# Kernel optimization log

Measured on AMD Instinct MI355X. Metric: run time of the kernel, lower is better.

Reference implementation:

```python
import jax, jax.numpy as jnp
import numpy as np

N, F, E, G = 50000, 128, 1600000, 64
CH = [16, 32, 64, 128, 256]
K = 3
EPS = 1e-5


def setup_inputs() -> dict:
    key = jax.random.key(0)
    ks = jax.random.split(key, 16)
    inp = {}
    inp["x"] = jax.random.normal(ks[0], (N, F), jnp.float32)
    inp["edge_weight"] = jax.random.uniform(ks[1], (E,), jnp.float32)
    inp["edge_index"] = jax.random.randint(ks[2], (2, E), 0, N)
    inp["batch_index"] = jnp.sort(jax.random.randint(ks[3], (N,), 0, G))
    dims = [F] + CH
    i = 4
    for l in range(5):
        fi, fo = dims[l], dims[l + 1]
        inp[f"W{l+1}"] = jax.random.normal(ks[i], (K, fi, fo), jnp.float32) / np.sqrt(K * fi)
        i += 1
        inp[f"b{l+1}"] = jnp.zeros((fo,), jnp.float32)
        if l < 4:  # no BN after the 5th conv
            inp[f"g{l+1}"] = jnp.ones((fo,), jnp.float32)
            inp[f"be{l+1}"] = jnp.zeros((fo,), jnp.float32)
    inp["Wd"] = jax.random.normal(ks[i], (2 * CH[-1], 4), jnp.float32) / np.sqrt(2 * CH[-1])
    inp["bd"] = jnp.zeros((4,), jnp.float32)
    inp["num_graphs"] = G
    return inp


def _bn(h, g, b):
    m = jnp.mean(h, axis=0)
    v = jnp.mean(jnp.square(h - m), axis=0)  # biased variance (torch training mode)
    return g * (h - m) / jnp.sqrt(v + EPS) + b


def reference(x, edge_weight, W1, b1, g1, be1, W2, b2, g2, be2, W3, b3, g3, be3,
              W4, b4, g4, be4, W5, b5, Wd, bd, edge_index, batch_index, num_graphs):
    n = x.shape[0]
    row, col = edge_index[0], edge_index[1]
    # sym-normalized Laplacian, lambda_max=2 -> scaled L_hat has zero diagonal,
    # off-diagonal = -w * deg^-1/2[row] * deg^-1/2[col]
    deg = jax.ops.segment_sum(edge_weight, row, num_segments=n)
    dinv = jnp.where(deg > 0, jax.lax.rsqrt(jnp.where(deg > 0, deg, 1.0)), 0.0)
    norm = -edge_weight * dinv[row] * dinv[col]

    def prop(z):  # L_hat @ z via sparse gather/scatter over edges
        return jax.ops.segment_sum(norm[:, None] * z[col], row, num_segments=n)

    def cheb(z, W, b):  # T0=z, T1=L z, T2=2 L T1 - T0
        t1 = prop(z)
        out = z @ W[0] + t1 @ W[1]
        t2 = 2.0 * prop(t1) - z
        return out + t2 @ W[2] + b

    h = _bn(jax.nn.softplus(cheb(x, W1, b1)), g1, be1)
    h = _bn(jax.nn.softplus(cheb(h, W2, b2)), g2, be2)
    h = _bn(jax.nn.softplus(cheb(h, W3, b3)), g3, be3)
    h = _bn(jax.nn.softplus(cheb(h, W4, b4)), g4, be4)
    h = cheb(h, W5, b5)

    mx = jax.ops.segment_max(h, batch_index, num_segments=num_graphs)
    mx = jnp.where(jnp.isfinite(mx), mx, 0.0)  # guard empty segments
    cnt = jax.ops.segment_sum(jnp.ones((n,), h.dtype), batch_index, num_segments=num_graphs)
    mean = jax.ops.segment_sum(h, batch_index, num_segments=num_graphs) / jnp.maximum(cnt, 1.0)[:, None]
    pooled = jnp.concatenate([mx, mean], axis=1)  # [G, 512]
    logits = pooled @ Wd + bd
    return jax.nn.log_softmax(logits, axis=-1)
```

## Files before the change

kernel.cpp:

```cpp
#include <hip/hip_runtime.h>
#include <cmath>

#define NN 50000
#define NE 1600000
#define NG 64
#define CAP 96

typedef __attribute__((ext_vector_type(8))) short short8_t;
typedef __attribute__((ext_vector_type(4))) float floatx4;
typedef __attribute__((ext_vector_type(4))) unsigned short us4;

static __device__ __forceinline__ float softplusf(float x) {
    return fmaxf(x, 0.0f) + log1pf(expf(-fabsf(x)));
}

static __device__ __forceinline__ float bf2f(unsigned short u) {
    return __uint_as_float(((unsigned)u) << 16);
}
static __device__ __forceinline__ unsigned short f2bf(float x) {
    unsigned u = __float_as_uint(x);
    unsigned t = (u >> 16) & 1u;
    return (unsigned short)((u + 0x7FFFu + t) >> 16);
}

static __device__ __forceinline__ void split_bf16(float x, unsigned short& hi, unsigned short& lo) {
    unsigned u = __float_as_uint(x);
    unsigned hb = u & 0xFFFF0000u;
    hi = (unsigned short)(hb >> 16);
    float r = x - __uint_as_float(hb);
    lo = f2bf(r);
}

__global__ void k_slot(const int* __restrict__ row, const int* __restrict__ col,
                       const float* __restrict__ w,
                       int* __restrict__ cnt, int2* __restrict__ slots) {
    int e = blockIdx.x * blockDim.x + threadIdx.x;
    if (e < NE) {
        int r = row[e];
        int k = atomicAdd(&cnt[r], 1);
        k = min(k, CAP - 1);
        slots[(size_t)r * CAP + k] = make_int2(col[e], __float_as_int(w[e]));
    }
}

__global__ __launch_bounds__(256) void k_degsum(const int* __restrict__ cnt,
                                                const int2* __restrict__ slots,
                                                float* __restrict__ dinv) {
    int tid = threadIdx.x;
    int lane = tid & 15;
    int node = blockIdx.x * 16 + (tid >> 4);
    if (node >= NN) return;
    int e = cnt[node];
    const int2* base = slots + (size_t)node * CAP;
    float s = 0.0f;
    for (int k = lane; k < e; k += 16) s += __int_as_float(base[k].y);
#pragma unroll
    for (int m = 8; m >= 1; m >>= 1) s += __shfl_xor(s, m);
    if (lane == 0) dinv[node] = (s > 0.0f) ? rsqrtf(s) : 0.0f;
}

__global__ __launch_bounds__(256) void k_rescale(const int* __restrict__ cnt,
                                                 int2* __restrict__ slots,
                                                 const float* __restrict__ dinv) {
    int tid = threadIdx.x;
    int lane = tid & 15;
    int node = blockIdx.x * 16 + (tid >> 4);
    if (node >= NN) return;
    int e = cnt[node];
    float dr = dinv[node];
    int2* base = slots + (size_t)node * CAP;
    for (int k = lane; k < e; k += 16) {
        int2 s = base[k];
        float wv = __int_as_float(s.y);
        base[k].y = __float_as_int(-wv * dr * dinv[s.x]);
    }
}

__global__ void k_wcat1(const float* __restrict__ W1, float* __restrict__ wc) {
    int i = blockIdx.x * blockDim.x + threadIdx.x;
    if (i < 128 * 48) {
        int k = i / 48, j = i - k * 48;
        float v;
        if (j < 16)      v = W1[k * 16 + j] - W1[2 * 2048 + k * 16 + j];
        else if (j < 32) v = W1[2048 + k * 16 + (j - 16)];
        else             v = W1[2 * 2048 + k * 16 + (j - 32)];
        wc[i] = v;
    }
}

__global__ void k_wsplit(const float* __restrict__ W, int K, int N,
                         unsigned short* __restrict__ hiT, unsigned short* __restrict__ loT) {
    int idx = blockIdx.x * 256 + threadIdx.x;
    if (idx < K * N) {
        int k = idx / N, n = idx - k * N;
        unsigned short h, l;
        split_bf16(W[idx], h, l);
        hiT[(size_t)n * K + k] = h;
        loT[(size_t)n * K + k] = l;
    }
}

#define ASTR 40

__global__ __launch_bounds__(256, 2) void k_gemm_mfma_f32A(
    const float* __restrict__ A, int lda,
    const unsigned short* __restrict__ BhiT,
    const unsigned short* __restrict__ BloT,
    unsigned short* __restrict__ C, int ldc,
    int M, int K, int Ncol)
{
    __shared__ unsigned short Ah[128 * ASTR];
    __shared__ unsigned short Al[128 * ASTR];
    __shared__ unsigned short Bh[128 * ASTR];
    __shared__ unsigned short Bl[128 * ASTR];

    const int tid = threadIdx.x;
    const int lane = tid & 63;
    const int wave = tid >> 6;
    const int wm = wave >> 1, wn = wave & 1;
    const int quad = lane >> 4, l16 = lane & 15;
    const int bm = blockIdx.y * 128, bn = blockIdx.x * 128;
    const int srow = tid >> 1;
    const int skq  = (tid & 1) * 16;

    floatx4 acc[4][4];
#pragma unroll
    for (int i = 0; i < 4; ++i)
#pragma unroll
        for (int j = 0; j < 4; ++j) acc[i][j] = (floatx4){0.f, 0.f, 0.f, 0.f};

    for (int k0 = 0; k0 < K; k0 += 32) {
        float4 a0 = make_float4(0, 0, 0, 0), a1 = a0, a2 = a0, a3 = a0;
        const int ga = bm + srow;
        if (ga < M) {
            const float* Ap = A + (size_t)ga * lda + k0 + skq;
            a0 = *(const float4*)(Ap + 0);
            a1 = *(const float4*)(Ap + 4);
            a2 = *(const float4*)(Ap + 8);
            a3 = *(const float4*)(Ap + 12);
        }
        uint4 bh0 = make_uint4(0, 0, 0, 0), bh1 = bh0, bl0 = bh0, bl1 = bh0;
        const int gb = bn + srow;
        if (gb < Ncol) {
            const unsigned short* ph = BhiT + (size_t)gb * K + k0 + skq;
            const unsigned short* pl = BloT + (size_t)gb * K + k0 + skq;
            bh0 = *(const uint4*)(ph);
            bh1 = *(const uint4*)(ph + 8);
            bl0 = *(const uint4*)(pl);
            bl1 = *(const uint4*)(pl + 8);
        }
        __attribute__((aligned(16))) unsigned short ah[16], al[16];
        const float av[16] = {a0.x, a0.y, a0.z, a0.w, a1.x, a1.y, a1.z, a1.w,
                              a2.x, a2.y, a2.z, a2.w, a3.x, a3.y, a3.z, a3.w};
#pragma unroll
        for (int i = 0; i < 16; ++i) split_bf16(av[i], ah[i], al[i]);

        __syncthreads();
        *(uint4*)&Ah[srow * ASTR + skq]     = *(const uint4*)&ah[0];
        *(uint4*)&Ah[srow * ASTR + skq + 8] = *(const uint4*)&ah[8];
        *(uint4*)&Al[srow * ASTR + skq]     = *(const uint4*)&al[0];
        *(uint4*)&Al[srow * ASTR + skq + 8] = *(const uint4*)&al[8];
        *(uint4*)&Bh[srow * ASTR + skq]     = bh0;
        *(uint4*)&Bh[srow * ASTR + skq + 8] = bh1;
        *(uint4*)&Bl[srow * ASTR + skq]     = bl0;
        *(uint4*)&Bl[srow * ASTR + skq + 8] = bl1;
        __syncthreads();

        short8_t afh[4], afl[4], bfh[4], bfl[4];
#pragma unroll
        for (int t = 0; t < 4; ++t) {
            const int m = wm * 64 + t * 16 + l16;
            afh[t] = *(const short8_t*)&Ah[m * ASTR + quad * 8];
            afl[t] = *(const short8_t*)&Al[m * ASTR + quad * 8];
            const int n = wn * 64 + t * 16 + l16;
            bfh[t] = *(const short8_t*)&Bh[n * ASTR + quad * 8];
            bfl[t] = *(const short8_t*)&Bl[n * ASTR + quad * 8];
        }
#pragma unroll
        for (int i = 0; i < 4; ++i)
#pragma unroll
            for (int j = 0; j < 4; ++j) {
                acc[i][j] = __builtin_amdgcn_mfma_f32_16x16x32_bf16(afh[i], bfh[j], acc[i][j], 0, 0, 0);
                acc[i][j] = __builtin_amdgcn_mfma_f32_16x16x32_bf16(afh[i], bfl[j], acc[i][j], 0, 0, 0);
                acc[i][j] = __builtin_amdgcn_mfma_f32_16x16x32_bf16(afl[i], bfh[j], acc[i][j], 0, 0, 0);
            }
    }

#pragma unroll
    for (int j = 0; j < 4; ++j) {
        const int col = bn + wn * 64 + j * 16 + l16;
        if (col >= Ncol) continue;
#pragma unroll
        for (int i = 0; i < 4; ++i) {
#pragma unroll
            for (int r = 0; r < 4; ++r) {
                const int row = bm + wm * 64 + i * 16 + quad * 4 + r;
                if (row >= M) continue;
                C[(size_t)row * ldc + col] = f2bf(acc[i][j][r]);
            }
        }
    }
}

__global__ __launch_bounds__(256, 2) void k_gemm_mfma_bf(
    const unsigned short* __restrict__ A, int lda,
    const unsigned short* __restrict__ BhiT,
    const unsigned short* __restrict__ BloT,
    void* __restrict__ Cv, int ldc,
    int M, int K, int Ncol,
    const float* __restrict__ bias, int act, int c_f32)
{
    __shared__ unsigned short Ah[128 * ASTR];
    __shared__ unsigned short Bh[128 * ASTR];
    __shared__ unsigned short Bl[128 * ASTR];

    const int tid = threadIdx.x;
    const int lane = tid & 63;
    const int wave = tid >> 6;
    const int wm = wave >> 1, wn = wave & 1;
    const int quad = lane >> 4, l16 = lane & 15;
    const int bm = blockIdx.y * 128, bn = blockIdx.x * 128;
    const int srow = tid >> 1;
    const int skq  = (tid & 1) * 16;

    floatx4 acc[4][4];
#pragma unroll
    for (int i = 0; i < 4; ++i)
#pragma unroll
        for (int j = 0; j < 4; ++j) acc[i][j] = (floatx4){0.f, 0.f, 0.f, 0.f};

    for (int k0 = 0; k0 < K; k0 += 32) {
        uint4 a0 = make_uint4(0, 0, 0, 0), a1 = a0;
        const int ga = bm + srow;
        if (ga < M) {
            const unsigned short* Ap = A + (size_t)ga * lda + k0 + skq;
            a0 = *(const uint4*)(Ap);
            a1 = *(const uint4*)(Ap + 8);
        }
        uint4 bh0 = make_uint4(0, 0, 0, 0), bh1 = bh0, bl0 = bh0, bl1 = bh0;
        const int gb = bn + srow;
        if (gb < Ncol) {
            const unsigned short* ph = BhiT + (size_t)gb * K + k0 + skq;
            const unsigned short* pl = BloT + (size_t)gb * K + k0 + skq;
            bh0 = *(const uint4*)(ph);
            bh1 = *(const uint4*)(ph + 8);
            bl0 = *(const uint4*)(pl);
            bl1 = *(const uint4*)(pl + 8);
        }
        __syncthreads();
        *(uint4*)&Ah[srow * ASTR + skq]     = a0;
        *(uint4*)&Ah[srow * ASTR + skq + 8] = a1;
        *(uint4*)&Bh[srow * ASTR + skq]     = bh0;
        *(uint4*)&Bh[srow * ASTR + skq + 8] = bh1;
        *(uint4*)&Bl[srow * ASTR + skq]     = bl0;
        *(uint4*)&Bl[srow * ASTR + skq + 8] = bl1;
        __syncthreads();

        short8_t afh[4], bfh[4], bfl[4];
#pragma unroll
        for (int t = 0; t < 4; ++t) {
            const int m = wm * 64 + t * 16 + l16;
            afh[t] = *(const short8_t*)&Ah[m * ASTR + quad * 8];
            const int n = wn * 64 + t * 16 + l16;
            bfh[t] = *(const short8_t*)&Bh[n * ASTR + quad * 8];
            bfl[t] = *(const short8_t*)&Bl[n * ASTR + quad * 8];
        }
#pragma unroll
        for (int i = 0; i < 4; ++i)
#pragma unroll
            for (int j = 0; j < 4; ++j) {
                acc[i][j] = __builtin_amdgcn_mfma_f32_16x16x32_bf16(afh[i], bfh[j], acc[i][j], 0, 0, 0);
                acc[i][j] = __builtin_amdgcn_mfma_f32_16x16x32_bf16(afh[i], bfl[j], acc[i][j], 0, 0, 0);
            }
    }

    float* Cf = (float*)Cv;
    unsigned short* Cb = (unsigned short*)Cv;
#pragma unroll
    for (int j = 0; j < 4; ++j) {
        const int col = bn + wn * 64 + j * 16 + l16;
        if (col >= Ncol) continue;
        const float bv = bias ? bias[col] : 0.0f;
#pragma unroll
        for (int i = 0; i < 4; ++i) {
#pragma unroll
            for (int r = 0; r < 4; ++r) {
                const int row = bm + wm * 64 + i * 16 + quad * 4 + r;
                if (row >= M) continue;
                float v = acc[i][j][r] + bv;
                if (act) v = softplusf(v);
                if (c_f32) Cf[(size_t)row * ldc + col] = v;
                else       Cb[(size_t)row * ldc + col] = f2bf(v);
            }
        }
    }
}

__global__ __launch_bounds__(256) void k_gemm(
    const unsigned short* __restrict__ A, int lda,
    const float* __restrict__ B, int ldb,
    unsigned short* __restrict__ C, int ldc,
    int M, int K, int Ncol,
    const float* __restrict__ bias, int act)
{
    __shared__ float As[16][128];
    __shared__ float Bs[16][128];
    const int tid = threadIdx.x;
    const int tx = tid & 15;
    const int ty = tid >> 4;
    const int bm = blockIdx.y * 128;
    const int bn = blockIdx.x * 128;
    const int arow = tid >> 1;
    const int akq = (tid & 1) * 8;
    const int bkr = tid >> 4;
    const int bcq = (tid & 15) * 8;

    float acc[8][8];
#pragma unroll
    for (int i = 0; i < 8; ++i)
#pragma unroll
        for (int j = 0; j < 8; ++j) acc[i][j] = 0.0f;

    for (int k0 = 0; k0 < K; k0 += 16) {
        uint4 ald = make_uint4(0, 0, 0, 0);
        int gr = bm + arow;
        if (gr < M) ald = *(const uint4*)(A + (size_t)gr * lda + k0 + akq);
        float4 b0 = make_float4(0, 0, 0, 0), b1 = make_float4(0, 0, 0, 0);
        int cb = bn + bcq;
        const float* Bp = B + (k0 + bkr) * ldb;
        if (cb < Ncol)     b0 = *(const float4*)(Bp + cb);
        if (cb + 4 < Ncol) b1 = *(const float4*)(Bp + cb + 4);
        __syncthreads();
        const unsigned short* au = (const unsigned short*)&ald;
#pragma unroll
        for (int i = 0; i < 8; ++i) As[akq + i][arow] = bf2f(au[i]);
        *(float4*)&Bs[bkr][bcq] = b0;
        *(float4*)&Bs[bkr][bcq + 4] = b1;
        __syncthreads();
#pragma unroll
        for (int kk = 0; kk < 16; ++kk) {
            float a[8], b[8];
            float4 t;
            t = *(const float4*)&As[kk][ty * 4];      a[0] = t.x; a[1] = t.y; a[2] = t.z; a[3] = t.w;
            t = *(const float4*)&As[kk][64 + ty * 4]; a[4] = t.x; a[5] = t.y; a[6] = t.z; a[7] = t.w;
            t = *(const float4*)&Bs[kk][tx * 4];      b[0] = t.x; b[1] = t.y; b[2] = t.z; b[3] = t.w;
            t = *(const float4*)&Bs[kk][64 + tx * 4]; b[4] = t.x; b[5] = t.y; b[6] = t.z; b[7] = t.w;
#pragma unroll
            for (int i = 0; i < 8; ++i)
#pragma unroll
                for (int j = 0; j < 8; ++j)
                    acc[i][j] = fmaf(a[i], b[j], acc[i][j]);
        }
    }
#pragma unroll
    for (int i = 0; i < 8; ++i) {
        int r = bm + ((i < 4) ? (ty * 4 + i) : (64 + ty * 4 + i - 4));
        if (r >= M) continue;
#pragma unroll
        for (int j = 0; j < 8; ++j) {
            int cl = bn + ((j < 4) ? (tx * 4 + j) : (64 + tx * 4 + j - 4));
            if (cl >= Ncol) continue;
            float v = acc[i][j];
            if (bias) v += bias[cl];
            if (act) v = softplusf(v);
            C[(size_t)r * ldc + cl] = f2bf(v);
        }
    }
}

__global__ __launch_bounds__(256) void k_prop(
    const int* __restrict__ cnt, const int2* __restrict__ slots,
    const unsigned short* __restrict__ z, int zld, int zoff,
    unsigned short* __restrict__ out, int outld, int ooff,
    int ltw, float alpha,
    const unsigned short* __restrict__ add1, int a1ld, int a1off, float c1,
    const unsigned short* __restrict__ add2, int a2ld, int a2off,
    const float* __restrict__ bias, int act)
{
    const int T = 1 << ltw;
    const int lane = threadIdx.x & (T - 1);
    const int node = blockIdx.x * (256 >> ltw) + (threadIdx.x >> ltw);
    if (node >= NN) return;
    const int f4 = lane * 4;
    const int e = cnt[node];
    const int2* base = slots + (size_t)node * CAP;
    float ax = 0, ay = 0, az = 0, aw = 0;
    float bx = 0, by = 0, bz = 0, bw = 0;
    const unsigned short* zp = z + zoff + f4;
    int p = 0;
    for (; p + 4 <= e; p += 4) {
        int2 s0 = base[p + 0], s1 = base[p + 1], s2 = base[p + 2], s3 = base[p + 3];
        float w0 = __int_as_float(s0.y), w1 = __int_as_float(s1.y);
        float w2 = __int_as_float(s2.y), w3 = __int_as_float(s3.y);
        const us4 z0 = *(const us4*)(zp + (size_t)s0.x * zld);
        const us4 z1 = *(const us4*)(zp + (size_t)s1.x * zld);
        const us4 z2 = *(const us4*)(zp + (size_t)s2.x * zld);
        const us4 z3 = *(const us4*)(zp + (size_t)s3.x * zld);
        ax = fmaf(w0, bf2f(z0.x), ax); ay = fmaf(w0, bf2f(z0.y), ay);
        az = fmaf(w0, bf2f(z0.z), az); aw = fmaf(w0, bf2f(z0.w), aw);
        bx = fmaf(w1, bf2f(z1.x), bx); by = fmaf(w1, bf2f(z1.y), by);
        bz = fmaf(w1, bf2f(z1.z), bz); bw = fmaf(w1, bf2f(z1.w), bw);
        ax = fmaf(w2, bf2f(z2.x), ax); ay = fmaf(w2, bf2f(z2.y), ay);
        az = fmaf(w2, bf2f(z2.z), az); aw = fmaf(w2, bf2f(z2.w), aw);
        bx = fmaf(w3, bf2f(z3.x), bx); by = fmaf(w3, bf2f(z3.y), by);
        bz = fmaf(w3, bf2f(z3.z), bz); bw = fmaf(w3, bf2f(z3.w), bw);
    }
    for (; p < e; ++p) {
        int2 s = base[p];
        float wv = __int_as_float(s.y);
        const us4 zv = *(const us4*)(zp + (size_t)s.x * zld);
        ax = fmaf(wv, bf2f(zv.x), ax); ay = fmaf(wv, bf2f(zv.y), ay);
        az = fmaf(wv, bf2f(zv.z), az); aw = fmaf(wv, bf2f(zv.w), aw);
    }
    ax += bx; ay += by; az += bz; aw += bw;
    ax *= alpha; ay *= alpha; az *= alpha; aw *= alpha;
    if (add1) {
        const us4 t = *(const us4*)(add1 + (size_t)node * a1ld + a1off + f4);
        ax = fmaf(c1, bf2f(t.x), ax); ay = fmaf(c1, bf2f(t.y), ay);
        az = fmaf(c1, bf2f(t.z), az); aw = fmaf(c1, bf2f(t.w), aw);
    }
    if (add2) {
        const us4 t = *(const us4*)(add2 + (size_t)node * a2ld + a2off + f4);
        ax += bf2f(t.x); ay += bf2f(t.y); az += bf2f(t.z); aw += bf2f(t.w);
    }
    if (bias) {
        const float4 t = *(const float4*)(bias + f4);
        ax += t.x; ay += t.y; az += t.z; aw += t.w;
    }
    if (act) { ax = softplusf(ax); ay = softplusf(ay); az = softplusf(az); aw = softplusf(aw); }
    us4 o;
    o.x = f2bf(ax); o.y = f2bf(ay); o.z = f2bf(az); o.w = f2bf(aw);
    *(us4*)(out + (size_t)node * outld + ooff + f4) = o;
}

__global__ __launch_bounds__(256) void k_bnstats(const unsigned short* __restrict__ h, int ld, int lc,
                                                 float* __restrict__ stats) {
    const int C = 1 << lc;
    const int tid = threadIdx.x;
    const int c = tid & (C - 1);
    const int rpb = 256 >> lc;
    int r = blockIdx.x * rpb + (tid >> lc);
    const int stride = gridDim.x * rpb;
    float s = 0.0f, q = 0.0f;
    for (; r < NN; r += stride) {
        float v = bf2f(h[(size_t)r * ld + c]);
        s += v;
        q = fmaf(v, v, q);
    }
    __shared__ float shs[256], shq[256];
    shs[tid] = s; shq[tid] = q;
    __syncthreads();
    for (int o = 128; o >= C; o >>= 1) {
        if (tid < o) { shs[tid] += shs[tid + o]; shq[tid] += shq[tid + o]; }
        __syncthreads();
    }
    if (tid < C) {
        atomicAdd(&stats[c], shs[tid]);
        atomicAdd(&stats[128 + c], shq[tid]);
    }
}

__global__ void k_bnapply(unsigned short* __restrict__ h, int ld, int lc,
                          const float* __restrict__ stats,
                          const float* __restrict__ g, const float* __restrict__ be) {
    int idx = blockIdx.x * 256 + threadIdx.x;
    if (idx >= (NN << lc)) return;
    int c = idx & ((1 << lc) - 1);
    int r = idx >> lc;
    const float invN = 1.0f / (float)NN;
    float m = stats[c] * invN;
    float var = fmaf(stats[128 + c], invN, -m * m);
    var = fmaxf(var, 0.0f);
    float inv = rsqrtf(var + 1e-5f);
    float v = bf2f(h[(size_t)r * ld + c]);
    h[(size_t)r * ld + c] = f2bf(fmaf(g[c] * inv, v - m, be[c]));
}

static __device__ __forceinline__ int lower_bound_dev(const int* __restrict__ b, int val) {
    int lo = 0, hi = NN;
    while (lo < hi) {
        int mid = (lo + hi) >> 1;
        if (b[mid] < val) lo = mid + 1; else hi = mid;
    }
    return lo;
}

__global__ void k_gbounds(const int* __restrict__ batch, int* __restrict__ gb) {
    int g = threadIdx.x;
    if (g <= NG) gb[g] = (g == NG) ? NN : lower_bound_dev(batch, g);
}

__global__ __launch_bounds__(256) void k_pool1(const float* __restrict__ h,
                                               const int* __restrict__ gb,
                                               float* __restrict__ partial) {
    int g = blockIdx.y;
    int j = blockIdx.x;
    int start = gb[g], end = gb[g + 1];
    int len = end - start;
    int chunk = (len + 15) >> 4;
    int s = start + j * chunk;
    int e = min(s + chunk, end);
    int c = threadIdx.x;
    float mx = -INFINITY, sum = 0.0f;
    for (int r = s; r < e; ++r) {
        float v = h[(size_t)r * 256 + c];
        mx = fmaxf(mx, v);
        sum += v;
    }
    size_t base = ((size_t)(g * 16 + j)) * 512;
    partial[base + c] = mx;
    partial[base + 256 + c] = sum;
}

__global__ __launch_bounds__(256) void k_pool2d(const float* __restrict__ partial,
                                                const int* __restrict__ gb,
                                                const float* __restrict__ Wd,
                                                const float* __restrict__ bd,
                                                float* __restrict__ out) {
    __shared__ float pl[512];
    __shared__ float red[4][256];
    int g = blockIdx.x;
    int c = threadIdx.x;
    float mx = -INFINITY, sum = 0.0f;
#pragma unroll
    for (int j = 0; j < 16; ++j) {
        size_t base = ((size_t)(g * 16 + j)) * 512;
        mx = fmaxf(mx, partial[base + c]);
        sum += partial[base + 256 + c];
    }
    int len = gb[g + 1] - gb[g];
    pl[c] = (len > 0) ? mx : 0.0f;
    pl[256 + c] = sum / fmaxf((float)len, 1.0f);
    __syncthreads();
    float p[4] = {0, 0, 0, 0};
    for (int k = c; k < 512; k += 256) {
        float pv = pl[k];
#pragma unroll
        for (int cc = 0; cc < 4; ++cc) p[cc] = fmaf(pv, Wd[k * 4 + cc], p[cc]);
    }
#pragma unroll
    for (int cc = 0; cc < 4; ++cc) red[cc][c] = p[cc];
    __syncthreads();
    for (int o = 128; o >= 1; o >>= 1) {
        if (c < o) {
#pragma unroll
            for (int cc = 0; cc < 4; ++cc) red[cc][c] += red[cc][c + o];
        }
        __syncthreads();
    }
    if (c == 0) {
        float l0 = red[0][0] + bd[0], l1 = red[1][0] + bd[1];
        float l2 = red[2][0] + bd[2], l3 = red[3][0] + bd[3];
        float m = fmaxf(fmaxf(l0, l1), fmaxf(l2, l3));
        float ls = m + logf(expf(l0 - m) + expf(l1 - m) + expf(l2 - m) + expf(l3 - m));
        out[g * 4 + 0] = l0 - ls;
        out[g * 4 + 1] = l1 - ls;
        out[g * 4 + 2] = l2 - ls;
        out[g * 4 + 3] = l3 - ls;
    }
}

extern "C" void kernel_launch(void* const* d_in, const int* in_sizes, int n_in,
                              void* d_out, int out_size, void* d_ws, size_t ws_size,
                              hipStream_t stream)
{
    const float* x    = (const float*)d_in[0];
    const float* ew   = (const float*)d_in[1];
    const int*   row  = (const int*)d_in[2];
    const int*   colp = row + NE;
    const int*   batch = (const int*)d_in[3];
    const float* W1 = (const float*)d_in[4];
    const float* b1 = (const float*)d_in[5];
    const float* g1 = (const float*)d_in[6];
    const float* be1 = (const float*)d_in[7];
    const float* W2 = (const float*)d_in[8];
    const float* b2 = (const float*)d_in[9];
    const float* g2 = (const float*)d_in[10];
    const float* be2 = (const float*)d_in[11];
    const float* W3 = (const float*)d_in[12];
    const float* b3 = (const float*)d_in[13];
    const float* g3 = (const float*)d_in[14];
    const float* be3 = (const float*)d_in[15];
    const float* W4 = (const float*)d_in[16];
    const float* b4 = (const float*)d_in[17];
    const float* g4 = (const float*)d_in[18];
    const float* be4 = (const float*)d_in[19];
    const float* W5 = (const float*)d_in[20];
    const float* b5 = (const float*)d_in[21];
    const float* Wd = (const float*)d_in[22];
    const float* bd = (const float*)d_in[23];
    float* outp = (float*)d_out;
    (void)in_sizes; (void)n_in; (void)out_size; (void)ws_size; (void)ew;

    char* wsb = (char*)d_ws;
    size_t off = 0;
    auto take = [&](size_t bytes) -> void* {
        void* p = wsb + off;
        off = (off + bytes + 255) & ~(size_t)255;
        return p;
    };
    int*   cnt    = (int*)take((size_t)NN * sizeof(int));
    float* dinv   = (float*)take((size_t)NN * sizeof(float));
    int*   gb     = (int*)take((NG + 1) * sizeof(int));
    int2*  slots  = (int2*)take((size_t)NN * CAP * sizeof(int2));
    float* statsA = (float*)take(4 * 256 * sizeof(float));
    float* wcat   = (float*)take(6144 * sizeof(float));
    unsigned short* bt1h = (unsigned short*)take(48 * 128 * 2);
    unsigned short* bt1l = (unsigned short*)take(48 * 128 * 2);
    unsigned short* bt3h = (unsigned short*)take(64 * 96 * 2);
    unsigned short* bt3l = (unsigned short*)take(64 * 96 * 2);
    unsigned short* bt4h = (unsigned short*)take(128 * 192 * 2);
    unsigned short* bt4l = (unsigned short*)take(128 * 192 * 2);
    unsigned short* bt5h = (unsigned short*)take(256 * 384 * 2);
    unsigned short* bt5l = (unsigned short*)take(256 * 384 * 2);
    float* partial= (float*)take((size_t)NG * 16 * 512 * sizeof(float));
    unsigned short* P   = (unsigned short*)take((size_t)NN * 48 * 2);
    unsigned short* uv  = (unsigned short*)take((size_t)NN * 32 * 2);
    unsigned short* Hc2 = (unsigned short*)take((size_t)NN * 48 * 2);
    unsigned short* Hc3 = (unsigned short*)take((size_t)NN * 96 * 2);
    unsigned short* Hc4 = (unsigned short*)take((size_t)NN * 192 * 2);
    unsigned short* Hc5 = (unsigned short*)take((size_t)NN * 384 * 2);
    float* h5   = (float*)take((size_t)NN * 256 * sizeof(float));

    float* stats1 = statsA;
    float* stats2 = statsA + 256;
    float* stats3 = statsA + 512;
    float* stats4 = statsA + 768;

    hipMemsetAsync(cnt, 0, NN * sizeof(int), stream);
    hipMemsetAsync(statsA, 0, 4 * 256 * sizeof(float), stream);

    k_slot<<<6250, 256, 0, stream>>>(row, colp, ew, cnt, slots);
    k_degsum<<<3125, 256, 0, stream>>>(cnt, slots, dinv);
    k_rescale<<<3125, 256, 0, stream>>>(cnt, slots, dinv);

    k_wcat1<<<24, 256, 0, stream>>>(W1, wcat);
    k_gbounds<<<1, 128, 0, stream>>>(batch, gb);
    k_wsplit<<<24, 256, 0, stream>>>(wcat, 128, 48, bt1h, bt1l);
    k_wsplit<<<24, 256, 0, stream>>>(W3, 96, 64, bt3h, bt3l);
    k_wsplit<<<96, 256, 0, stream>>>(W4, 192, 128, bt4h, bt4l);
    k_wsplit<<<384, 256, 0, stream>>>(W5, 384, 256, bt5h, bt5l);

    k_gemm_mfma_f32A<<<dim3(1, 391), 256, 0, stream>>>(x, 128, bt1h, bt1l, P, 48, NN, 128, 48);
    k_prop<<<1563, 256, 0, stream>>>(cnt, slots, P, 48, 16, uv, 32, 0, 3, 1.0f,
                                     nullptr, 0, 0, 0.0f, nullptr, 0, 0, nullptr, 0);
    k_prop<<<782, 256, 0, stream>>>(cnt, slots, uv, 32, 16, Hc2, 48, 0, 2, 2.0f,
                                    P, 48, 0, 1.0f, uv, 32, 0, b1, 1);
    k_bnstats<<<256, 256, 0, stream>>>(Hc2, 48, 4, stats1);
    k_bnapply<<<3125, 256, 0, stream>>>(Hc2, 48, 4, stats1, g1, be1);

    k_prop<<<782, 256, 0, stream>>>(cnt, slots, Hc2, 48, 0, Hc2, 48, 16, 2, 1.0f,
                                    nullptr, 0, 0, 0.0f, nullptr, 0, 0, nullptr, 0);
    k_prop<<<782, 256, 0, stream>>>(cnt, slots, Hc2, 48, 16, Hc2, 48, 32, 2, 2.0f,
                                    Hc2, 48, 0, -1.0f, nullptr, 0, 0, nullptr, 0);
    k_gemm<<<dim3(1, 391), 256, 0, stream>>>(Hc2, 48, W2, 32, Hc3, 96, NN, 48, 32, b2, 1);
    k_bnstats<<<256, 256, 0, stream>>>(Hc3, 96, 5, stats2);
    k_bnapply<<<6250, 256, 0, stream>>>(Hc3, 96, 5, stats2, g2, be2);

    k_prop<<<1563, 256, 0, stream>>>(cnt, slots, Hc3, 96, 0, Hc3, 96, 32, 3, 1.0f,
                                     nullptr, 0, 0, 0.0f, nullptr, 0, 0, nullptr, 0);
    k_prop<<<1563, 256, 0, stream>>>(cnt, slots, Hc3, 96, 32, Hc3, 96, 64, 3, 2.0f,
                                     Hc3, 96, 0, -1.0f, nullptr, 0, 0, nullptr, 0);
    k_gemm_mfma_bf<<<dim3(1, 391), 256, 0, stream>>>(Hc3, 96, bt3h, bt3l, Hc4, 192, NN, 96, 64, b3, 1, 0);
    k_bnstats<<<256, 256, 0, stream>>>(Hc4, 192, 6, stats3);
    k_bnapply<<<12500, 256, 0, stream>>>(Hc4, 192, 6, stats3, g3, be3);

    k_prop<<<3125, 256, 0, stream>>>(cnt, slots, Hc4, 192, 0, Hc4, 192, 64, 4, 1.0f,
                                     nullptr, 0, 0, 0.0f, nullptr, 0, 0, nullptr, 0);
    k_prop<<<3125, 256, 0, stream>>>(cnt, slots, Hc4, 192, 64, Hc4, 192, 128, 4, 2.0f,
                                     Hc4, 192, 0, -1.0f, nullptr, 0, 0, nullptr, 0);
    k_gemm_mfma_bf<<<dim3(1, 391), 256, 0, stream>>>(Hc4, 192, bt4h, bt4l, Hc5, 384, NN, 192, 128, b4, 1, 0);
    k_bnstats<<<256, 256, 0, stream>>>(Hc5, 384, 7, stats4);
    k_bnapply<<<25000, 256, 0, stream>>>(Hc5, 384, 7, stats4, g4, be4);

    k_prop<<<6250, 256, 0, stream>>>(cnt, slots, Hc5, 384, 0, Hc5, 384, 128, 5, 1.0f,
                                     nullptr, 0, 0, 0.0f, nullptr, 0, 0, nullptr, 0);
    k_prop<<<6250, 256, 0, stream>>>(cnt, slots, Hc5, 384, 128, Hc5, 384, 256, 5, 2.0f,
                                     Hc5, 384, 0, -1.0f, nullptr, 0, 0, nullptr, 0);
    k_gemm_mfma_bf<<<dim3(2, 391), 256, 0, stream>>>(Hc5, 384, bt5h, bt5l, h5, 256, NN, 384, 256, b5, 0, 1);

    k_pool1<<<dim3(16, 64), 256, 0, stream>>>(h5, gb, partial);
    k_pool2d<<<64, 256, 0, stream>>>(partial, gb, Wd, bd, outp);
}
```

Baseline: 874.3 us.

## Pack edge slots into 32-bit index+fp16 weight and widen prop lanes to 8 features

```diff
diff --git a/kernel.cpp b/kernel.cpp
--- a/kernel.cpp
+++ b/kernel.cpp
@@ -1,4 +1,5 @@
 #include <hip/hip_runtime.h>
+#include <hip/hip_fp16.h>
 #include <cmath>
 
 #define NN 50000
@@ -8,7 +9,7 @@
 
 typedef __attribute__((ext_vector_type(8))) short short8_t;
 typedef __attribute__((ext_vector_type(4))) float floatx4;
-typedef __attribute__((ext_vector_type(4))) unsigned short us4;
+typedef __attribute__((ext_vector_type(8))) unsigned short us8;
 
 static __device__ __forceinline__ float softplusf(float x) {
     return fmaxf(x, 0.0f) + log1pf(expf(-fabsf(x)));
@@ -21,6 +22,14 @@
     unsigned u = __float_as_uint(x);
     unsigned t = (u >> 16) & 1u;
     return (unsigned short)((u + 0x7FFFu + t) >> 16);
+}
+static __device__ __forceinline__ float h2f(unsigned u) {
+    __half_raw r; r.x = (unsigned short)(u & 0xFFFFu);
+    return __half2float(__half(r));
+}
+static __device__ __forceinline__ unsigned short f2h(float x) {
+    __half h = __float2half_rn(x);
+    return static_cast<__half_raw>(h).x;
 }
 
 static __device__ __forceinline__ void split_bf16(float x, unsigned short& hi, unsigned short& lo) {
@@ -59,20 +68,22 @@
     if (lane == 0) dinv[node] = (s > 0.0f) ? rsqrtf(s) : 0.0f;
 }
 
-__global__ __launch_bounds__(256) void k_rescale(const int* __restrict__ cnt,
-                                                 int2* __restrict__ slots,
-                                                 const float* __restrict__ dinv) {
+__global__ __launch_bounds__(256) void k_repack(const int* __restrict__ cnt,
+                                                const int2* __restrict__ slots,
+                                                const float* __restrict__ dinv,
+                                                unsigned* __restrict__ pslots) {
     int tid = threadIdx.x;
     int lane = tid & 15;
     int node = blockIdx.x * 16 + (tid >> 4);
     if (node >= NN) return;
     int e = cnt[node];
     float dr = dinv[node];
-    int2* base = slots + (size_t)node * CAP;
+    const int2* base = slots + (size_t)node * CAP;
+    unsigned* pb = pslots + (size_t)node * CAP;
     for (int k = lane; k < e; k += 16) {
         int2 s = base[k];
-        float wv = __int_as_float(s.y);
-        base[k].y = __float_as_int(-wv * dr * dinv[s.x]);
+        float wv = -__int_as_float(s.y) * dr * dinv[s.x];
+        pb[k] = ((unsigned)s.x << 16) | (unsigned)f2h(wv);
     }
 }
 
@@ -369,7 +380,7 @@
 }
 
 __global__ __launch_bounds__(256) void k_prop(
-    const int* __restrict__ cnt, const int2* __restrict__ slots,
+    const int* __restrict__ cnt, const unsigned* __restrict__ pslots,
     const unsigned short* __restrict__ z, int zld, int zoff,
     unsigned short* __restrict__ out, int outld, int ooff,
     int ltw, float alpha,
@@ -381,56 +392,61 @@
     const int lane = threadIdx.x & (T - 1);
     const int node = blockIdx.x * (256 >> ltw) + (threadIdx.x >> ltw);
     if (node >= NN) return;
-    const int f4 = lane * 4;
+    const int f8 = lane * 8;
     const int e = cnt[node];
-    const int2* base = slots + (size_t)node * CAP;
-    float ax = 0, ay = 0, az = 0, aw = 0;
-    float bx = 0, by = 0, bz = 0, bw = 0;
-    const unsigned short* zp = z + zoff + f4;
+    const unsigned* base = pslots + (size_t)node * CAP;
+    float accA[8] = {0, 0, 0, 0, 0, 0, 0, 0};
+    float accB[8] = {0, 0, 0, 0, 0, 0, 0, 0};
+    const unsigned short* zp = z + zoff + f8;
     int p = 0;
     for (; p + 4 <= e; p += 4) {
-        int2 s0 = base[p + 0], s1 = base[p + 1], s2 = base[p + 2], s3 = base[p + 3];
-        float w0 = __int_as_float(s0.y), w1 = __int_as_float(s1.y);
-        float w2 = __int_as_float(s2.y), w3 = __int_as_float(s3.y);
-        const us4 z0 = *(const us4*)(zp + (size_t)s0.x * zld);
-        const us4 z1 = *(const us4*)(zp + (size_t)s1.x * zld);
-        const us4 z2 = *(const us4*)(zp + (size_t)s2.x * zld);
-        const us4 z3 = *(const us4*)(zp + (size_t)s3.x * zld);
-        ax = fmaf(w0, bf2f(z0.x), ax); ay = fmaf(w0, bf2f(z0.y), ay);
-        az = fmaf(w0, bf2f(z0.z), az); aw = fmaf(w0, bf2f(z0.w), aw);
-        bx = fmaf(w1, bf2f(z1.x), bx); by = fmaf(w1, bf2f(z1.y), by);
-        bz = fmaf(w1, bf2f(z1.z), bz); bw = fmaf(w1, bf2f(z1.w), bw);
-        ax = fmaf(w2, bf2f(z2.x), ax); ay = fmaf(w2, bf2f(z2.y), ay);
-        az = fmaf(w2, bf2f(z2.z), az); aw = fmaf(w2, bf2f(z2.w), aw);
-        bx = fmaf(w3, bf2f(z3.x), bx); by = fmaf(w3, bf2f(z3.y), by);
-        bz = fmaf(w3, bf2f(z3.z), bz); bw = fmaf(w3, bf2f(z3.w), bw);
+        unsigned s0 = base[p + 0], s1 = base[p + 1], s2 = base[p + 2], s3 = base[p + 3];
+        float w0 = h2f(s0), w1 = h2f(s1), w2 = h2f(s2), w3 = h2f(s3);
+        const us8 z0 = *(const us8*)(zp + (size_t)(s0 >> 16) * zld);
+        const us8 z1 = *(const us8*)(zp + (size_t)(s1 >> 16) * zld);
+        const us8 z2 = *(const us8*)(zp + (size_t)(s2 >> 16) * zld);
+        const us8 z3 = *(const us8*)(zp + (size_t)(s3 >> 16) * zld);
+#pragma unroll
+        for (int i = 0; i < 8; ++i) {
+            accA[i] = fmaf(w0, bf2f(z0[i]), accA[i]);
+            accB[i] = fmaf(w1, bf2f(z1[i]), accB[i]);
+            accA[i] = fmaf(w2, bf2f(z2[i]), accA[i]);
+            accB[i] = fmaf(w3, bf2f(z3[i]), accB[i]);
+        }
     }
     for (; p < e; ++p) {
-        int2 s = base[p];
-        float wv = __int_as_float(s.y);
-        const us4 zv = *(const us4*)(zp + (size_t)s.x * zld);
-        ax = fmaf(wv, bf2f(zv.x), ax); ay = fmaf(wv, bf2f(zv.y), ay);
-        az = fmaf(wv, bf2f(zv.z), az); aw = fmaf(wv, bf2f(zv.w), aw);
-    }
-    ax += bx; ay += by; az += bz; aw += bw;
-    ax *= alpha; ay *= alpha; az *= alpha; aw *= alpha;
+        unsigned s = base[p];
+        float wv = h2f(s);
+        const us8 zv = *(const us8*)(zp + (size_t)(s >> 16) * zld);
+#pragma unroll
+        for (int i = 0; i < 8; ++i) accA[i] = fmaf(wv, bf2f(zv[i]), accA[i]);
+    }
+#pragma unroll
+    for (int i = 0; i < 8; ++i) accA[i] = alpha * (accA[i] + accB[i]);
     if (add1) {
-        const us4 t = *(const us4*)(add1 + (size_t)node * a1ld + a1off + f4);
-        ax = fmaf(c1, bf2f(t.x), ax); ay = fmaf(c1, bf2f(t.y), ay);
-        az = fmaf(c1, bf2f(t.z), az); aw = fmaf(c1, bf2f(t.w), aw);
+        const us8 t = *(const us8*)(add1 + (size_t)node * a1ld + a1off + f8);
+#pragma unroll
+        for (int i = 0; i < 8; ++i) accA[i] = fmaf(c1, bf2f(t[i]), accA[i]);
     }
     if (add2) {
-        const us4 t = *(const us4*)(add2 + (size_t)node * a2ld + a2off + f4);
-        ax += bf2f(t.x); ay += bf2f(t.y); az += bf2f(t.z); aw += bf2f(t.w);
+        const us8 t = *(const us8*)(add2 + (size_t)node * a2ld + a2off + f8);
+#pragma unroll
+        for (int i = 0; i < 8; ++i) accA[i] += bf2f(t[i]);
     }
     if (bias) {
-        const float4 t = *(const float4*)(bias + f4);
-        ax += t.x; ay += t.y; az += t.z; aw += t.w;
-    }
-    if (act) { ax = softplusf(ax); ay = softplusf(ay); az = softplusf(az); aw = softplusf(aw); }
-    us4 o;
-    o.x = f2bf(ax); o.y = f2bf(ay); o.z = f2bf(az); o.w = f2bf(aw);
-    *(us4*)(out + (size_t)node * outld + ooff + f4) = o;
+        const float4 t0 = *(const float4*)(bias + f8);
+        const float4 t1 = *(const float4*)(bias + f8 + 4);
+        accA[0] += t0.x; accA[1] += t0.y; accA[2] += t0.z; accA[3] += t0.w;
+        accA[4] += t1.x; accA[5] += t1.y; accA[6] += t1.z; accA[7] += t1.w;
+    }
+    if (act) {
+#pragma unroll
+        for (int i = 0; i < 8; ++i) accA[i] = softplusf(accA[i]);
+    }
+    us8 o;
+#pragma unroll
+    for (int i = 0; i < 8; ++i) o[i] = f2bf(accA[i]);
+    *(us8*)(out + (size_t)node * outld + ooff + f8) = o;
 }
 
 __global__ __launch_bounds__(256) void k_bnstats(const unsigned short* __restrict__ h, int ld, int lc,
@@ -603,6 +619,7 @@
     float* dinv   = (float*)take((size_t)NN * sizeof(float));
     int*   gb     = (int*)take((NG + 1) * sizeof(int));
     int2*  slots  = (int2*)take((size_t)NN * CAP * sizeof(int2));
+    unsigned* pslots = (unsigned*)take((size_t)NN * CAP * sizeof(unsigned));
     float* statsA = (float*)take(4 * 256 * sizeof(float));
     float* wcat   = (float*)take(6144 * sizeof(float));
     unsigned short* bt1h = (unsigned short*)take(48 * 128 * 2);
@@ -632,7 +649,7 @@
 
     k_slot<<<6250, 256, 0, stream>>>(row, colp, ew, cnt, slots);
     k_degsum<<<3125, 256, 0, stream>>>(cnt, slots, dinv);
-    k_rescale<<<3125, 256, 0, stream>>>(cnt, slots, dinv);
+    k_repack<<<3125, 256, 0, stream>>>(cnt, slots, dinv, pslots);
 
     k_wcat1<<<24, 256, 0, stream>>>(W1, wcat);
     k_gbounds<<<1, 128, 0, stream>>>(batch, gb);
@@ -642,40 +659,40 @@
     k_wsplit<<<384, 256, 0, stream>>>(W5, 384, 256, bt5h, bt5l);
 
     k_gemm_mfma_f32A<<<dim3(1, 391), 256, 0, stream>>>(x, 128, bt1h, bt1l, P, 48, NN, 128, 48);
-    k_prop<<<1563, 256, 0, stream>>>(cnt, slots, P, 48, 16, uv, 32, 0, 3, 1.0f,
-                                     nullptr, 0, 0, 0.0f, nullptr, 0, 0, nullptr, 0);
-    k_prop<<<782, 256, 0, stream>>>(cnt, slots, uv, 32, 16, Hc2, 48, 0, 2, 2.0f,
+    k_prop<<<782, 256, 0, stream>>>(cnt, pslots, P, 48, 16, uv, 32, 0, 2, 1.0f,
+                                    nullptr, 0, 0, 0.0f, nullptr, 0, 0, nullptr, 0);
+    k_prop<<<391, 256, 0, stream>>>(cnt, pslots, uv, 32, 16, Hc2, 48, 0, 1, 2.0f,
                                     P, 48, 0, 1.0f, uv, 32, 0, b1, 1);
     k_bnstats<<<256, 256, 0, stream>>>(Hc2, 48, 4, stats1);
     k_bnapply<<<3125, 256, 0, stream>>>(Hc2, 48, 4, stats1, g1, be1);
 
-    k_prop<<<782, 256, 0, stream>>>(cnt, slots, Hc2, 48, 0, Hc2, 48, 16, 2, 1.0f,
+    k_prop<<<391, 256, 0, stream>>>(cnt, pslots, Hc2, 48, 0, Hc2, 48, 16, 1, 1.0f,
                                     nullptr, 0, 0, 0.0f, nullptr, 0, 0, nullptr, 0);
-    k_prop<<<782, 256, 0, stream>>>(cnt, slots, Hc2, 48, 16, Hc2, 48, 32, 2, 2.0f,
+    k_prop<<<391, 256, 0, stream>>>(cnt, pslots, Hc2, 48, 16, Hc2, 48, 32, 1, 2.0f,
                                     Hc2, 48, 0, -1.0f, nullptr, 0, 0, nullptr, 0);
     k_gemm<<<dim3(1, 391), 256, 0, stream>>>(Hc2, 48, W2, 32, Hc3, 96, NN, 48, 32, b2, 1);
     k_bnstats<<<256, 256, 0, stream>>>(Hc3, 96, 5, stats2);
     k_bnapply<<<6250, 256, 0, stream>>>(Hc3, 96, 5, stats2, g2, be2);
 
-    k_prop<<<1563, 256, 0, stream>>>(cnt, slots, Hc3, 96, 0, Hc3, 96, 32, 3, 1.0f,
-                                     nullptr, 0, 0, 0.0f, nullptr, 0, 0, nullptr, 0);
-    k_prop<<<1563, 256, 0, stream>>>(cnt, slots, Hc3, 96, 32, Hc3, 96, 64, 3, 2.0f,
-                                     Hc3, 96, 0, -1.0f, nullptr, 0, 0, nullptr, 0);
+    k_prop<<<782, 256, 0, stream>>>(cnt, pslots, Hc3, 96, 0, Hc3, 96, 32, 2, 1.0f,
+                                    nullptr, 0, 0, 0.0f, nullptr, 0, 0, nullptr, 0);
+    k_prop<<<782, 256, 0, stream>>>(cnt, pslots, Hc3, 96, 32, Hc3, 96, 64, 2, 2.0f,
+                                    Hc3, 96, 0, -1.0f, nullptr, 0, 0, nullptr, 0);
     k_gemm_mfma_bf<<<dim3(1, 391), 256, 0, stream>>>(Hc3, 96, bt3h, bt3l, Hc4, 192, NN, 96, 64, b3, 1, 0);
     k_bnstats<<<256, 256, 0, stream>>>(Hc4, 192, 6, stats3);
     k_bnapply<<<12500, 256, 0, stream>>>(Hc4, 192, 6, stats3, g3, be3);
 
-    k_prop<<<3125, 256, 0, stream>>>(cnt, slots, Hc4, 192, 0, Hc4, 192, 64, 4, 1.0f,
+    k_prop<<<1563, 256, 0, stream>>>(cnt, pslots, Hc4, 192, 0, Hc4, 192, 64, 3, 1.0f,
                                      nullptr, 0, 0, 0.0f, nullptr, 0, 0, nullptr, 0);
-    k_prop<<<3125, 256, 0, stream>>>(cnt, slots, Hc4, 192, 64, Hc4, 192, 128, 4, 2.0f,
+    k_prop<<<1563, 256, 0, stream>>>(cnt, pslots, Hc4, 192, 64, Hc4, 192, 128, 3, 2.0f,
                                      Hc4, 192, 0, -1.0f, nullptr, 0, 0, nullptr, 0);
     k_gemm_mfma_bf<<<dim3(1, 391), 256, 0, stream>>>(Hc4, 192, bt4h, bt4l, Hc5, 384, NN, 192, 128, b4, 1, 0);
     k_bnstats<<<256, 256, 0, stream>>>(Hc5, 384, 7, stats4);
     k_bnapply<<<25000, 256, 0, stream>>>(Hc5, 384, 7, stats4, g4, be4);
 
-    k_prop<<<6250, 256, 0, stream>>>(cnt, slots, Hc5, 384, 0, Hc5, 384, 128, 5, 1.0f,
+    k_prop<<<3125, 256, 0, stream>>>(cnt, pslots, Hc5, 384, 0, Hc5, 384, 128, 4, 1.0f,
                                      nullptr, 0, 0, 0.0f, nullptr, 0, 0, nullptr, 0);
-    k_prop<<<6250, 256, 0, stream>>>(cnt, slots, Hc5, 384, 128, Hc5, 384, 256, 5, 2.0f,
+    k_prop<<<3125, 256, 0, stream>>>(cnt, pslots, Hc5, 384, 128, Hc5, 384, 256, 4, 2.0f,
                                      Hc5, 384, 0, -1.0f, nullptr, 0, 0, nullptr, 0);
     k_gemm_mfma_bf<<<dim3(2, 391), 256, 0, stream>>>(Hc5, 384, bt5h, bt5l, h5, 256, NN, 384, 256, b5, 0, 1);
 
```

After: 1.028 ms. 17.6% more time.
